# Performance work log

Measured on AMD Instinct MI355X. Metric: run time of the kernel, lower is better.

Reference implementation:

```python
import jax, jax.numpy as jnp
import numpy as np

N, F_IN, HID, NCLS, E = 100000, 256, 256, 32, 3200000
NHEADS, HDIM, MFEAT = 4, 64, 266  # MFEAT = int(HDIM * ln(HDIM)), performer default
ALPHA, KSTEPS, EPS = 0.1, 10, 1e-4


def setup_inputs() -> dict:
    key = jax.random.key(0)
    ks = jax.random.split(key, 16)
    p = lambda k, sh: (jax.random.normal(k, sh, dtype=jnp.float32) * 0.02)
    return {
        "x": jax.random.normal(ks[0], (N, F_IN), dtype=jnp.float32),
        "edge_index": jax.random.randint(ks[1], (2, E), 0, N, dtype=jnp.int64),
        "lin1_w": p(ks[2], (HID, F_IN)), "lin1_b": p(ks[3], (HID,)),
        "lin2_w": p(ks[4], (NCLS, 2 * HID)), "lin2_b": p(ks[5], (NCLS,)),
        "q_w": p(ks[6], (HID, F_IN)), "q_b": p(ks[7], (HID,)),
        "k_w": p(ks[8], (HID, F_IN)), "k_b": p(ks[9], (HID,)),
        "v_w": p(ks[10], (HID, F_IN)), "v_b": p(ks[11], (HID,)),
        "proj": jax.random.normal(ks[12], (MFEAT, HDIM), dtype=jnp.float32),
    }


def _softmax_kernel(data, proj, is_query):
    # performer_pytorch softmax random-feature map
    d = data.shape[-1]
    m = proj.shape[0]
    dn = d ** -0.25
    ratio = m ** -0.5
    data_dash = jnp.einsum('bhnd,md->bhnm', data * dn, proj)
    diag = 0.5 * (dn ** 2) * jnp.sum(data * data, axis=-1, keepdims=True)  # [b,h,n,1]
    if is_query:
        mx = jax.lax.stop_gradient(jnp.max(data_dash, axis=-1, keepdims=True))
    else:
        mx = jax.lax.stop_gradient(jnp.max(data_dash, axis=(-2, -1), keepdims=True))
    return ratio * (jnp.exp(data_dash - diag - mx) + EPS)


def _fast_attention(q, k, v, proj):
    # non-causal performer linear attention; q,k,v: [b,h,n,d]
    qp = _softmax_kernel(q, proj, True)   # [b,h,n,m]
    kp = _softmax_kernel(k, proj, False)  # [b,h,n,m]
    k_sum = jnp.sum(kp, axis=-2)                                   # [b,h,m]
    d_inv = 1.0 / jnp.einsum('bhnm,bhm->bhn', qp, k_sum)           # [b,h,n]
    context = jnp.einsum('bhnm,bhnd->bhmd', kp, v)                 # [b,h,m,d]
    return jnp.einsum('bhmd,bhnm,bhn->bhnd', context, qp, d_inv)   # [b,h,n,d]


def _appnp(x, edge_index, n):
    # gcn_norm with self-loops, then K iterations of x <- (1-a) A_hat x + a h
    src = jnp.concatenate([edge_index[0], jnp.arange(n, dtype=edge_index.dtype)])
    dst = jnp.concatenate([edge_index[1], jnp.arange(n, dtype=edge_index.dtype)])
    deg = jax.ops.segment_sum(jnp.ones_like(dst, dtype=x.dtype), dst, num_segments=n)
    dis = jnp.where(deg > 0, jax.lax.rsqrt(deg), 0.0)
    w = (dis[src] * dis[dst])[:, None]  # [E+N, 1]
    h = x
    for _ in range(KSTEPS):
        msg = jax.ops.segment_sum(x[src] * w, dst, num_segments=n)
        x = (1.0 - ALPHA) * msg + ALPHA * h
    return x


def reference(x, edge_index, lin1_w, lin1_b, lin2_w, lin2_b,
              q_w, q_b, k_w, k_b, v_w, v_b, proj):
    n = x.shape[0]
    # dropout layers are identity in eval mode
    xu = x[None]  # [1, N, F]
    q = (xu @ q_w.T + q_b).reshape(1, n, NHEADS, HDIM).transpose(0, 2, 1, 3)
    k = (xu @ k_w.T + k_b).reshape(1, n, NHEADS, HDIM).transpose(0, 2, 1, 3)
    v = (xu @ v_w.T + v_b).reshape(1, n, NHEADS, HDIM).transpose(0, 2, 1, 3)
    attn = _fast_attention(q, k, v, proj)                      # [1,h,n,d]
    trans = attn.transpose(0, 2, 1, 3).reshape(n, HID)         # [N, HID]
    gnn1 = x @ lin1_w.T + lin1_b                               # [N, HID]
    cat = jax.nn.elu(jnp.concatenate([gnn1, trans], axis=1))   # [N, 2*HID]
    gnn2 = jax.nn.elu(cat @ lin2_w.T + lin2_b)                 # [N, NCLS]
    final = _appnp(gnn2, edge_index, n)
    return jax.nn.log_softmax(final, axis=1), final
```

## Files before the change

kernel.cpp:

```cpp
#include <hip/hip_runtime.h>
#include <hip/hip_fp16.h>

#define NH 4
#define HD 64
#define MF 266
#define MP 288
#define NB 192
#define NBQ 128
#define DN 0.35355339059327373f
#define RATIO 0.06131393394849658f
#define EPSRF 1e-4f
#define REPS (RATIO*EPSRF)

typedef unsigned short u16;
typedef unsigned int u32;
typedef __attribute__((ext_vector_type(8))) short bf16x8;
typedef __attribute__((ext_vector_type(4))) float f32x4;
#define MFMA16(a,b,c) __builtin_amdgcn_mfma_f32_16x16x32_bf16(a,b,c,0,0,0)

__device__ __forceinline__ float bf2f(u16 u){ return __uint_as_float(((u32)u)<<16); }
__device__ __forceinline__ u16 f2bf(float f){ u32 u = __float_as_uint(f); u += 0x7FFFu + ((u>>16)&1u); return (u16)(u>>16); }
__device__ __forceinline__ u32 pack2bf(float a, float b){ return ((u32)f2bf(b)<<16) | f2bf(a); }
__device__ __forceinline__ float eluf(float x){ return x>0.f ? x : (expf(x)-1.f); }

__global__ void k_cvtw(const float* __restrict__ qw, const float* __restrict__ kw,
                       const float* __restrict__ vw, const float* __restrict__ lw,
                       const float* __restrict__ l2w, const float* __restrict__ proj,
                       u16* __restrict__ Wb, u16* __restrict__ projp, u16* __restrict__ l2wb){
  int i = blockIdx.x*256 + threadIdx.x;
  if (i < 262144){
    int sec = i>>16, r = i&65535;
    const float* s = sec==0?qw : sec==1?kw : sec==2?vw : lw;
    Wb[i] = f2bf(s[r]);
  }
  if (i < MP*64){
    int r = i>>6, c = i&63;
    projp[i] = f2bf(r < MF ? proj[r*64 + c] : 0.f);
  }
  if (i < 32*512) l2wb[i] = f2bf(l2w[i]);
}

__global__ __launch_bounds__(512,4) void k_proj(
    const float* __restrict__ x, const u16* __restrict__ Wb,
    const float* __restrict__ qb, const float* __restrict__ kb,
    const float* __restrict__ vb, const float* __restrict__ lb,
    u16* __restrict__ Q, u16* __restrict__ K, u16* __restrict__ V,
    u16* __restrict__ G1, int n)
{
  __shared__ u32 Xs[128*128];
  const int tid = threadIdx.x;
  const int w = tid>>6, l = tid&63;
  const int wr = w>>2, wc = w&3;
  const int lm = l&15, lk = l>>4;
  const int row0 = blockIdx.x*128;
  #pragma unroll 4
  for (int q=0;q<16;++q){
    int idx = q*512 + tid;
    int r = idx>>6, c4 = idx&63;
    int rr = row0 + r; if (rr > n-1) rr = n-1;
    float4 v = *(const float4*)(x + (size_t)rr*256 + c4*4);
    int word = (c4*2) ^ ((r&7)<<2);
    *(uint2*)&Xs[r*128 + word] = make_uint2(pack2bf(v.x,v.y), pack2bf(v.z,v.w));
  }
  __syncthreads();
  #pragma unroll 1
  for (int ct=0; ct<8; ++ct){
    const int c0 = ct*128 + wc*32;
    f32x4 acc[4][2] = {};
    #pragma unroll 2
    for (int kt=0; kt<8; ++kt){
      bf16x8 Af[4], Bf[2];
      #pragma unroll
      for (int jj=0;jj<2;jj++)
        Bf[jj] = *(const bf16x8*)(Wb + (size_t)(c0 + jj*16 + lm)*256 + kt*32 + lk*8);
      #pragma unroll
      for (int i=0;i<4;i++){
        const int rl = wr*64 + i*16 + lm;
        Af[i] = *(const bf16x8*)&Xs[rl*128 + ((kt*16 + lk*4) ^ ((rl&7)<<2))];
      }
      #pragma unroll
      for (int i=0;i<4;i++)
        #pragma unroll
        for (int jj=0;jj<2;jj++)
          acc[i][jj] = MFMA16(Af[i], Bf[jj], acc[i][jj]);
    }
    const int sel = c0>>8;
    const float* bp = sel==0?qb : sel==1?kb : sel==2?vb : lb;
    u16* d3 = sel==0?Q : sel==1?K : sel==2?V : G1;
    u32* dst32 = (u32*)d3;
    const bool even = (lm&1)==0;
    #pragma unroll
    for (int jj=0;jj<2;jj++){
      const int cc = (c0&255) + jj*16 + lm;
      const float bias = bp[cc];
      const int ccA = cc & ~1;
      const int hh = ccA>>6, dd = ccA&63;
      #pragma unroll
      for (int i=0;i<4;i++){
        const int rb = row0 + wr*64 + i*16 + lk*4;
        u32 m01 = pack2bf(acc[i][jj][0]+bias, acc[i][jj][1]+bias);
        u32 m23 = pack2bf(acc[i][jj][2]+bias, acc[i][jj][3]+bias);
        u32 oa = __shfl_xor(m01,1);
        u32 ob = __shfl_xor(m23,1);
        u32 wA = even ? ((m01 & 0xffffu) | ((oa & 0xffffu)<<16))
                      : ((ob  & 0xffffu) | ((m23 & 0xffffu)<<16));
        u32 wB = even ? ((m01 >> 16) | (oa & 0xffff0000u))
                      : ((ob  >> 16) | (m23 & 0xffff0000u));
        const int rA = rb + (even ? 0 : 2);
        const int rB = rA + 1;
        if (sel==3){
          if (rA < n) dst32[(size_t)rA*128 + (ccA>>1)] = wA;
          if (rB < n) dst32[(size_t)rB*128 + (ccA>>1)] = wB;
        } else {
          if (rA < n) dst32[(((size_t)hh*n + rA)<<5) + (dd>>1)] = wA;
          if (rB < n) dst32[(((size_t)hh*n + rB)<<5) + (dd>>1)] = wB;
        }
      }
    }
  }
}

__global__ void k_vcs(const u16* __restrict__ Vb, float* __restrict__ vcs, int n){
  const int h = blockIdx.y, tid = threadIdx.x;
  const int d = tid&63, seg = tid>>6;
  float s = 0.f;
  for (int node = blockIdx.x*4 + seg; node < n; node += 256)
    s += bf2f(Vb[(((size_t)h*n + node)<<6) + d]);
  __shared__ float sm[4][64];
  sm[seg][d] = s; __syncthreads();
  if (tid < 64){
    float t2 = sm[0][tid]+sm[1][tid]+sm[2][tid]+sm[3][tid];
    atomicAdd(vcs + h*64 + tid, t2);
  }
}

__global__ __launch_bounds__(256) void k_ctx(
    const u16* __restrict__ Kb, const u16* __restrict__ Vb,
    const u16* __restrict__ projp,
    float* __restrict__ ctxp, float* __restrict__ ksump,
    u32* __restrict__ kmaxg, int n)
{
  __shared__ u32 kpT[288*32];
  __shared__ u16 Vt[64][72];
  __shared__ float redk[4][288];
  const int tid = threadIdx.x;
  const int w = tid>>6, l = tid&63;
  const int bb = blockIdx.x;
  const int h = blockIdx.y;
  const int lm = l&15, lk = l>>4;
  f32x4 cacc[18] = {};
  float ksa[18] = {};
  float mreg = -3.0e38f;
  const int ntile = (n+63)>>6;
  #pragma unroll 1
  for (int t=bb; t<ntile; t+=NB){
    const int n0 = t*64;
    __syncthreads();
    #pragma unroll
    for (int q=0;q<2;q++){
      int e8 = tid + q*256;
      int nn = e8>>3, d0 = (e8&7)*8;
      uint4 rv = make_uint4(0,0,0,0);
      if (n0+nn < n) rv = *(const uint4*)(Vb + (((size_t)h*n + n0+nn)<<6) + d0);
      const u16* pv = (const u16*)&rv;
      #pragma unroll
      for (int s=0;s<8;s++) Vt[d0+s][nn] = pv[s];
    }
    int rr = n0 + w*16 + lm; if (rr > n-1) rr = n-1;
    const u16* Kbase = Kb + (((size_t)h*n + rr)<<6);
    bf16x8 af0 = *(const bf16x8*)(Kbase + lk*8);
    bf16x8 af1 = *(const bf16x8*)(Kbase + 32 + lk*8);
    float dg = 0.f;
    #pragma unroll
    for (int i2=0;i2<8;i2++){
      float a = bf2f(((const u16*)&af0)[i2]);
      float b = bf2f(((const u16*)&af1)[i2]);
      dg += a*a + b*b;
    }
    dg += __shfl_xor(dg,16); dg += __shfl_xor(dg,32);
    dg *= 0.0625f;
    float dgr[4];
    #pragma unroll
    for (int j=0;j<4;j++) dgr[j] = __shfl(dg, lk*4+j, 16);
    #pragma unroll
    for (int mt=0; mt<18; ++mt){
      bf16x8 b0 = *(const bf16x8*)(projp + (size_t)(mt*16+lm)*64 + lk*8);
      bf16x8 b1 = *(const bf16x8*)(projp + (size_t)(mt*16+lm)*64 + 32 + lk*8);
      f32x4 D = {0,0,0,0};
      D = MFMA16(af0, b0, D);
      D = MFMA16(af1, b1, D);
      const int m = mt*16 + lm;
      const bool vm = m < MF;
      float colsum = 0.f;
      u32 pk0 = 0, pk1 = 0;
      #pragma unroll
      for (int j=0;j<4;j++){
        float ddash = DN * D[j];
        float kp = 0.f;
        if (vm && (n0 + w*16 + lk*4 + j) < n){
          kp = RATIO * __expf(ddash - dgr[j]);
          mreg = fmaxf(mreg, ddash);
          colsum += kp;
        }
        if (j<2) pk0 |= ((u32)f2bf(kp)) << (16*j);
        else     pk1 |= ((u32)f2bf(kp)) << (16*(j-2));
      }
      const int wn0 = w*8 + lk*2;
      *(uint2*)&kpT[m*32 + (wn0 ^ ((m&7)<<2))] = make_uint2(pk0, pk1);
      colsum += __shfl_xor(colsum,16); colsum += __shfl_xor(colsum,32);
      ksa[mt] += colsum;
    }
    __syncthreads();
    #pragma unroll
    for (int mt=0; mt<18; ++mt){
      const int m = mt*16 + lm;
      #pragma unroll
      for (int ks=0;ks<2;++ks){
        bf16x8 a = *(const bf16x8*)&kpT[m*32 + ((ks*16 + lk*4) ^ ((m&7)<<2))];
        bf16x8 bv = *(const bf16x8*)&Vt[w*16+lm][ks*32 + lk*8];
        cacc[mt] = MFMA16(a, bv, cacc[mt]);
      }
    }
  }
  float* cp = ctxp + ((size_t)(h*NB + bb))*MP*64;
  #pragma unroll
  for (int mt=0;mt<18;++mt){
    #pragma unroll
    for (int j=0;j<4;j++){
      int m = mt*16 + lk*4 + j;
      cp[(size_t)m*64 + w*16 + lm] = cacc[mt][j];
    }
  }
  if (l < 16){
    #pragma unroll
    for (int mt=0;mt<18;++mt) redk[w][mt*16+lm] = ksa[mt];
  }
  __shared__ float redm[4];
  float mr = mreg;
  #pragma unroll
  for (int s=1;s<64;s<<=1) mr = fmaxf(mr, __shfl_xor(mr, s));
  if (l==0) redm[w] = mr;
  __syncthreads();
  for (int m2=tid; m2<MP; m2+=256){
    float s = redk[0][m2]+redk[1][m2]+redk[2][m2]+redk[3][m2];
    ksump[((size_t)(h*NB+bb))*MP + m2] = s;
  }
  if (tid==0){
    float bm = fmaxf(fmaxf(redm[0],redm[1]), fmaxf(redm[2],redm[3]));
    u32 b = __float_as_uint(bm);
    u32 enc = (b & 0x80000000u) ? ~b : (b | 0x80000000u);
    atomicMax(kmaxg + h, enc);
  }
}

__global__ void k_reduce(const float* __restrict__ ctxp, const float* __restrict__ ksump,
                         const u32* __restrict__ kmaxg, const float* __restrict__ vcs,
                         u16* __restrict__ ctxT, float* __restrict__ ksum, int n)
{
  const int T1 = NH*MP*64;
  int idx = blockIdx.x*256 + threadIdx.x;
  if (idx < T1){
    int h = idx/(MP*64), r = idx - h*MP*64, m = r>>6, d = r&63;
    u32 ee = kmaxg[h]; u32 b = (ee & 0x80000000u) ? (ee ^ 0x80000000u) : ~ee;
    float sc = __expf(-__uint_as_float(b));
    float s = 0.f;
    for (int bb=0; bb<NB; ++bb) s += ctxp[(((size_t)(h*NB+bb))*MP + m)*64 + d];
    float val = (m < MF) ? (sc*s + REPS*vcs[h*64 + d]) : 0.f;
    ctxT[((size_t)h*64 + d)*MP + m] = f2bf(val);
  } else if (idx < T1 + NH*MP){
    int k2 = idx - T1, h = k2/MP, m = k2 - h*MP;
    u32 ee = kmaxg[h]; u32 b = (ee & 0x80000000u) ? (ee ^ 0x80000000u) : ~ee;
    float sc = __expf(-__uint_as_float(b));
    float s = 0.f;
    for (int bb=0; bb<NB; ++bb) s += ksump[((size_t)(h*NB+bb))*MP + m];
    ksum[h*MP + m] = (m < MF) ? (sc*s + REPS*(float)n) : 0.f;
  }
}

__global__ __launch_bounds__(256) void k_qattn(
    const u16* __restrict__ Qb, const u16* __restrict__ projp,
    const u16* __restrict__ ctxT, const float* __restrict__ ksum,
    u16* __restrict__ trans, int n)
{
  __shared__ u32 pj[288*32];
  __shared__ u16 qp_lds[4][16][168];
  const int tid = threadIdx.x;
  const int w = tid>>6, l = tid&63;
  const int h = blockIdx.y;
  const int lm = l&15, lk = l>>4;
  #pragma unroll
  for (int q=0; q<9; ++q){
    int cix = q*256 + tid;
    int row = cix>>3, c4 = (cix&7)*4;
    uint4 v = *(const uint4*)(projp + row*64 + c4*2);
    *(uint4*)&pj[row*32 + (c4 ^ ((row&7)<<2))] = v;
  }
  float ksm[18];
  #pragma unroll
  for (int mt=0;mt<18;++mt) ksm[mt] = ksum[h*MP + mt*16 + lm];
  __syncthreads();
  const int ntile = (n+63)>>6;
  #pragma unroll 1
  for (int t = blockIdx.x; t < ntile; t += NBQ){
    const int nb = t*64 + w*16;
    int rr = nb + lm; if (rr > n-1) rr = n-1;
    const u16* Qbase = Qb + (((size_t)h*n + rr)<<6);
    bf16x8 af0 = *(const bf16x8*)(Qbase + lk*8);
    bf16x8 af1 = *(const bf16x8*)(Qbase + 32 + lk*8);
    float dg = 0.f;
    #pragma unroll
    for (int i2=0;i2<8;i2++){
      float a = bf2f(((const u16*)&af0)[i2]);
      float b = bf2f(((const u16*)&af1)[i2]);
      dg += a*a + b*b;
    }
    dg += __shfl_xor(dg,16); dg += __shfl_xor(dg,32);
    dg *= 0.0625f;
    float dgr[4];
    #pragma unroll
    for (int j=0;j<4;j++) dgr[j] = __shfl(dg, lk*4+j, 16);
    f32x4 D[18];
    #pragma unroll
    for (int mt=0;mt<18;++mt){
      const int m = mt*16 + lm;
      bf16x8 b0 = *(const bf16x8*)&pj[m*32 + ((lk*4) ^ ((m&7)<<2))];
      bf16x8 b1 = *(const bf16x8*)&pj[m*32 + ((16 + lk*4) ^ ((m&7)<<2))];
      f32x4 z = {0,0,0,0};
      z = MFMA16(af0, b0, z);
      z = MFMA16(af1, b1, z);
      D[mt] = z;
    }
    float rmax[4] = {-3.0e38f,-3.0e38f,-3.0e38f,-3.0e38f};
    #pragma unroll
    for (int mt=0;mt<17;++mt){
      const bool vm = (mt<16) || (lm<10);
      #pragma unroll
      for (int j=0;j<4;j++){
        float dd = DN*D[mt][j];
        if (vm) rmax[j] = fmaxf(rmax[j], dd);
      }
    }
    #pragma unroll
    for (int j=0;j<4;j++){
      #pragma unroll
      for (int s=1;s<16;s<<=1) rmax[j] = fmaxf(rmax[j], __shfl_xor(rmax[j], s));
    }
    float den[4] = {0,0,0,0};
    f32x4 o[4] = {{0,0,0,0},{0,0,0,0},{0,0,0,0},{0,0,0,0}};
    #pragma unroll
    for (int mt=0;mt<10;++mt){
      #pragma unroll
      for (int j=0;j<4;j++){
        float qp = RATIO*(__expf(DN*D[mt][j] - dgr[j] - rmax[j]) + EPSRF);
        den[j] += qp * ksm[mt];
        qp_lds[w][lk*4+j][mt*16+lm] = f2bf(qp);
      }
    }
    #pragma unroll
    for (int ks=0;ks<5;++ks){
      bf16x8 av = *(const bf16x8*)&qp_lds[w][lm][ks*32 + lk*8];
      #pragma unroll
      for (int dt=0;dt<4;++dt){
        bf16x8 bv = *(const bf16x8*)(ctxT + (size_t)(h*64 + dt*16 + lm)*MP + ks*32 + lk*8);
        o[dt] = MFMA16(av, bv, o[dt]);
      }
    }
    #pragma unroll
    for (int mt=10;mt<18;++mt){
      #pragma unroll
      for (int j=0;j<4;j++){
        float qp = RATIO*(__expf(DN*D[mt][j] - dgr[j] - rmax[j]) + EPSRF);
        den[j] += qp * ksm[mt];
        qp_lds[w][lk*4+j][(mt-10)*16+lm] = f2bf(qp);
      }
    }
    #pragma unroll
    for (int ks=5;ks<9;++ks){
      bf16x8 av = *(const bf16x8*)&qp_lds[w][lm][(ks-5)*32 + lk*8];
      #pragma unroll
      for (int dt=0;dt<4;++dt){
        bf16x8 bv = *(const bf16x8*)(ctxT + (size_t)(h*64 + dt*16 + lm)*MP + ks*32 + lk*8);
        o[dt] = MFMA16(av, bv, o[dt]);
      }
    }
    #pragma unroll
    for (int j=0;j<4;j++){
      #pragma unroll
      for (int s=1;s<16;s<<=1) den[j] += __shfl_xor(den[j], s);
    }
    #pragma unroll
    for (int j=0;j<4;j++){
      const int node = nb + lk*4 + j;
      if (node < n){
        const float dv = 1.f/den[j];
        #pragma unroll
        for (int dt=0;dt<4;++dt)
          trans[(size_t)node*256 + h*64 + dt*16 + lm] = f2bf(o[dt][j]*dv);
      }
    }
  }
}

__global__ __launch_bounds__(256) void k_gnn2(
    const u16* __restrict__ G1, const u16* __restrict__ trans,
    const u16* __restrict__ l2wb, const float* __restrict__ l2b,
    u16* __restrict__ xb0, int n)
{
  __shared__ u32 cat[64*256];
  const int tid = threadIdx.x;
  const int w = tid>>6, l = tid&63;
  const int lm = l&15, lk = l>>4;
  const int n0 = blockIdx.x*64;
  #pragma unroll
  for (int src=0; src<2; ++src){
    const u16* S = src ? trans : G1;
    #pragma unroll
    for (int q=0;q<8;++q){
      int idx = q*256 + tid;
      int row = idx>>5, v8 = idx&31;
      int rr = n0+row; if (rr > n-1) rr = n-1;
      uint4 raw = *(const uint4*)(S + (size_t)rr*256 + v8*8);
      const u16* p = (const u16*)&raw;
      u32 o2[4];
      #pragma unroll
      for (int t2=0;t2<4;++t2)
        o2[t2] = pack2bf(eluf(bf2f(p[t2*2])), eluf(bf2f(p[t2*2+1])));
      int word = (v8*4 + src*128) ^ ((row&7)<<2);
      *(uint4*)&cat[row*256 + word] = *(uint4*)o2;
    }
  }
  __syncthreads();
  f32x4 acc[2] = {{0,0,0,0},{0,0,0,0}};
  const int rowl = w*16 + lm;
  #pragma unroll 4
  for (int kt=0; kt<16; ++kt){
    bf16x8 a = *(const bf16x8*)&cat[rowl*256 + ((kt*16 + lk*4) ^ ((rowl&7)<<2))];
    #pragma unroll
    for (int jj=0;jj<2;++jj){
      bf16x8 b = *(const bf16x8*)(l2wb + (size_t)(jj*16+lm)*512 + kt*32 + lk*8);
      acc[jj] = MFMA16(a, b, acc[jj]);
    }
  }
  #pragma unroll
  for (int jj=0;jj<2;++jj){
    const int o = jj*16 + lm;
    const float bias = l2b[o];
    #pragma unroll
    for (int jr=0;jr<4;++jr){
      const int node = n0 + w*16 + lk*4 + jr;
      if (node < n)
        xb0[(size_t)node*32 + o] = f2bf(eluf(acc[jj][jr] + bias));
    }
  }
}

__global__ void k_edgemode(const int* __restrict__ ei, int* __restrict__ mode){
  __shared__ int any;
  if (threadIdx.x==0) any = 0;
  __syncthreads();
  if (ei[threadIdx.x*2+1] != 0) any = 1;
  __syncthreads();
  if (threadIdx.x==0) *mode = any;
}
__device__ __forceinline__ int edge_at(const int* ei, int mode, size_t idx){
  if (mode) return ei[idx];
  return (int)((const long long*)ei)[idx];
}

__global__ void k_hist(const int* __restrict__ ei, const int* __restrict__ mode,
                       u32* __restrict__ deg, int e){
  const int md = *mode;
  for (size_t i = (size_t)blockIdx.x*blockDim.x + threadIdx.x; i < (size_t)e; i += (size_t)gridDim.x*blockDim.x)
    atomicAdd(&deg[edge_at(ei, md, (size_t)e + i)], 1u);
}
__global__ void k_dis(const u32* __restrict__ deg, float* __restrict__ dis, int n){
  int i = blockIdx.x*256 + threadIdx.x;
  if (i<n) dis[i] = rsqrtf((float)(deg[i] + 1u));
}
__global__ __launch_bounds__(256) void k_bsum(const u32* __restrict__ deg,
                                              u32* __restrict__ bsum, int n){
  __shared__ u32 red[4];
  const int tid = threadIdx.x, lane = tid&63, wv = tid>>6;
  const int base = blockIdx.x*1024;
  u32 s = 0;
  #pragma unroll
  for (int q=0;q<4;++q){
    int i = base + q*256 + tid;
    if (i<n) s += deg[i];
  }
  #pragma unroll
  for (int off=1; off<64; off<<=1) s += __shfl_xor(s, off, 64);
  if (lane==0) red[wv] = s;
  __syncthreads();
  if (tid==0) bsum[blockIdx.x] = red[0]+red[1]+red[2]+red[3];
}
__global__ __launch_bounds__(1024) void k_bscan(u32* __restrict__ bsum,
                                                u32* __restrict__ rowp, int nblk){
  __shared__ u32 wsum[16];
  __shared__ u32 carry;
  const int tid = threadIdx.x, lane = tid&63, wv = tid>>6;
  if (tid==0){ carry = 0u; rowp[0] = 0u; }
  __syncthreads();
  for (int base=0; base<nblk; base+=1024){
    int i = base + tid;
    u32 v = (i<nblk)? bsum[i] : 0u;
    u32 s = v;
    #pragma unroll
    for (int off=1; off<64; off<<=1){
      u32 t = __shfl_up(s, off, 64);
      if (lane >= off) s += t;
    }
    if (lane==63) wsum[wv] = s;
    __syncthreads();
    if (wv==0){
      u32 ws = (lane<16)? wsum[lane] : 0u;
      #pragma unroll
      for (int off=1; off<16; off<<=1){
        u32 t = __shfl_up(ws, off, 64);
        if (lane >= off) ws += t;
      }
      if (lane<16) wsum[lane] = ws;
    }
    __syncthreads();
    if (i<nblk) bsum[i] = carry + (wv ? wsum[wv-1] : 0u) + s - v;
    __syncthreads();
    if (tid==0) carry += wsum[15];
    __syncthreads();
  }
}
__global__ __launch_bounds__(1024) void k_scan2(const u32* __restrict__ deg,
                                                const u32* __restrict__ bsum,
                                                u32* __restrict__ rowp, int n){
  __shared__ u32 wsum[16];
  const int tid = threadIdx.x, lane = tid&63, wv = tid>>6;
  const int i = blockIdx.x*1024 + tid;
  u32 v = (i<n)? deg[i] : 0u;
  u32 s = v;
  #pragma unroll
  for (int off=1; off<64; off<<=1){
    u32 t = __shfl_up(s, off, 64);
    if (lane >= off) s += t;
  }
  if (lane==63) wsum[wv] = s;
  __syncthreads();
  if (wv==0){
    u32 ws = (lane<16)? wsum[lane] : 0u;
    #pragma unroll
    for (int off=1; off<16; off<<=1){
      u32 t = __shfl_up(ws, off, 64);
      if (lane >= off) ws += t;
    }
    if (lane<16) wsum[lane] = ws;
  }
  __syncthreads();
  if (i<n) rowp[i+1] = bsum[blockIdx.x] + (wv ? wsum[wv-1] : 0u) + s;
}
__global__ void k_copy(const u32* __restrict__ a, u32* __restrict__ b, int n){
  int i = blockIdx.x*256 + threadIdx.x; if (i<n) b[i]=a[i];
}
__global__ void k_fill(const int* __restrict__ ei, const int* __restrict__ mode,
                       const float* __restrict__ dis,
                       u32* __restrict__ cur, uint2* __restrict__ cw, int e){
  const int md = *mode;
  for (size_t i = (size_t)blockIdx.x*blockDim.x + threadIdx.x; i < (size_t)e; i += (size_t)gridDim.x*blockDim.x){
    int s = edge_at(ei, md, i);
    int t = edge_at(ei, md, (size_t)e + i);
    u32 pos = atomicAdd(&cur[t], 1u);
    cw[pos] = make_uint2((u32)s, __float_as_uint(dis[s]*dis[t]));
  }
}

__global__ __launch_bounds__(256) void k_appnp(
    const u16* __restrict__ xin, const u16* __restrict__ hb16,
    u16* __restrict__ xout, const u32* __restrict__ rowp,
    const uint2* __restrict__ cw, const float* __restrict__ dis, int n)
{
  const int g = threadIdx.x>>3, j4 = threadIdx.x&7;
  const int node = blockIdx.x*32 + g;
  if (node >= n) return;
  const uint2* x64 = (const uint2*)xin;
  float d0 = dis[node];
  float dd = d0*d0;
  uint2 xv = x64[((size_t)node<<3) + j4];
  float a0 = dd*bf2f((u16)xv.x), a1 = dd*bf2f((u16)(xv.x>>16));
  float a2 = dd*bf2f((u16)xv.y), a3 = dd*bf2f((u16)(xv.y>>16));
  u32 r0 = rowp[node], r1 = rowp[node+1];
  u32 k = r0;
  for (; k+4 <= r1; k += 4){
    uint2 e0 = cw[k], e1 = cw[k+1], e2 = cw[k+2], e3 = cw[k+3];
    uint2 v0 = x64[((size_t)e0.x<<3)+j4], v1 = x64[((size_t)e1.x<<3)+j4];
    uint2 v2 = x64[((size_t)e2.x<<3)+j4], v3 = x64[((size_t)e3.x<<3)+j4];
    float w0=__uint_as_float(e0.y), w1=__uint_as_float(e1.y);
    float w2=__uint_as_float(e2.y), w3=__uint_as_float(e3.y);
    a0 += w0*bf2f((u16)v0.x) + w1*bf2f((u16)v1.x) + w2*bf2f((u16)v2.x) + w3*bf2f((u16)v3.x);
    a1 += w0*bf2f((u16)(v0.x>>16)) + w1*bf2f((u16)(v1.x>>16)) + w2*bf2f((u16)(v2.x>>16)) + w3*bf2f((u16)(v3.x>>16));
    a2 += w0*bf2f((u16)v0.y) + w1*bf2f((u16)v1.y) + w2*bf2f((u16)v2.y) + w3*bf2f((u16)v3.y);
    a3 += w0*bf2f((u16)(v0.y>>16)) + w1*bf2f((u16)(v1.y>>16)) + w2*bf2f((u16)(v2.y>>16)) + w3*bf2f((u16)(v3.y>>16));
  }
  for (; k < r1; ++k){
    uint2 e = cw[k];
    uint2 v = x64[((size_t)e.x<<3)+j4];
    float wgt = __uint_as_float(e.y);
    a0 += wgt*bf2f((u16)v.x);
    a1 += wgt*bf2f((u16)(v.x>>16));
    a2 += wgt*bf2f((u16)v.y);
    a3 += wgt*bf2f((u16)(v.y>>16));
  }
  uint2 hv = ((const uint2*)hb16)[((size_t)node<<3) + j4];
  uint2 o;
  o.x = pack2bf(0.9f*a0 + 0.1f*bf2f((u16)hv.x), 0.9f*a1 + 0.1f*bf2f((u16)(hv.x>>16)));
  o.y = pack2bf(0.9f*a2 + 0.1f*bf2f((u16)hv.y), 0.9f*a3 + 0.1f*bf2f((u16)(hv.y>>16)));
  ((uint2*)xout)[((size_t)node<<3) + j4] = o;
}

__global__ __launch_bounds__(256) void k_appnp_lsm(
    const u16* __restrict__ xin, const u16* __restrict__ hb16,
    float* __restrict__ out, const u32* __restrict__ rowp,
    const uint2* __restrict__ cw, const float* __restrict__ dis, int n)
{
  const int g = threadIdx.x>>3, j4 = threadIdx.x&7;
  const int node = blockIdx.x*32 + g;
  if (node >= n) return;
  const uint2* x64 = (const uint2*)xin;
  float d0 = dis[node];
  float dd = d0*d0;
  uint2 xv = x64[((size_t)node<<3) + j4];
  float a0 = dd*bf2f((u16)xv.x), a1 = dd*bf2f((u16)(xv.x>>16));
  float a2 = dd*bf2f((u16)xv.y), a3 = dd*bf2f((u16)(xv.y>>16));
  u32 r0 = rowp[node], r1 = rowp[node+1];
  u32 k = r0;
  for (; k+4 <= r1; k += 4){
    uint2 e0 = cw[k], e1 = cw[k+1], e2 = cw[k+2], e3 = cw[k+3];
    uint2 v0 = x64[((size_t)e0.x<<3)+j4], v1 = x64[((size_t)e1.x<<3)+j4];
    uint2 v2 = x64[((size_t)e2.x<<3)+j4], v3 = x64[((size_t)e3.x<<3)+j4];
    float w0=__uint_as_float(e0.y), w1=__uint_as_float(e1.y);
    float w2=__uint_as_float(e2.y), w3=__uint_as_float(e3.y);
    a0 += w0*bf2f((u16)v0.x) + w1*bf2f((u16)v1.x) + w2*bf2f((u16)v2.x) + w3*bf2f((u16)v3.x);
    a1 += w0*bf2f((u16)(v0.x>>16)) + w1*bf2f((u16)(v1.x>>16)) + w2*bf2f((u16)(v2.x>>16)) + w3*bf2f((u16)(v3.x>>16));
    a2 += w0*bf2f((u16)v0.y) + w1*bf2f((u16)v1.y) + w2*bf2f((u16)v2.y) + w3*bf2f((u16)v3.y);
    a3 += w0*bf2f((u16)(v0.y>>16)) + w1*bf2f((u16)(v1.y>>16)) + w2*bf2f((u16)(v2.y>>16)) + w3*bf2f((u16)(v3.y>>16));
  }
  for (; k < r1; ++k){
    uint2 e = cw[k];
    uint2 v = x64[((size_t)e.x<<3)+j4];
    float wgt = __uint_as_float(e.y);
    a0 += wgt*bf2f((u16)v.x);
    a1 += wgt*bf2f((u16)(v.x>>16));
    a2 += wgt*bf2f((u16)v.y);
    a3 += wgt*bf2f((u16)(v.y>>16));
  }
  uint2 hv = ((const uint2*)hb16)[((size_t)node<<3) + j4];
  float v0 = 0.9f*a0 + 0.1f*bf2f((u16)hv.x);
  float v1 = 0.9f*a1 + 0.1f*bf2f((u16)(hv.x>>16));
  float v2 = 0.9f*a2 + 0.1f*bf2f((u16)hv.y);
  float v3 = 0.9f*a3 + 0.1f*bf2f((u16)(hv.y>>16));
  float m = fmaxf(fmaxf(v0,v1), fmaxf(v2,v3));
  #pragma unroll
  for (int o2=1;o2<8;o2<<=1) m = fmaxf(m, __shfl_xor(m, o2, 8));
  float s = __expf(v0-m)+__expf(v1-m)+__expf(v2-m)+__expf(v3-m);
  #pragma unroll
  for (int o2=1;o2<8;o2<<=1) s += __shfl_xor(s, o2, 8);
  float ls = m + logf(s);
  float4 lsv = make_float4(v0-ls, v1-ls, v2-ls, v3-ls);
  *(float4*)(out + (size_t)node*32 + j4*4) = lsv;
  float4 raw = make_float4(v0, v1, v2, v3);
  *(float4*)(out + (size_t)n*32 + (size_t)node*32 + j4*4) = raw;
}

extern "C" void kernel_launch(void* const* d_in, const int* in_sizes, int n_in,
                              void* d_out, int out_size, void* d_ws, size_t ws_size,
                              hipStream_t stream)
{
  const float* x   = (const float*)d_in[0];
  const int*   ei  = (const int*)  d_in[1];
  const float* l1w = (const float*)d_in[2];
  const float* l1b = (const float*)d_in[3];
  const float* l2w = (const float*)d_in[4];
  const float* l2b = (const float*)d_in[5];
  const float* qw  = (const float*)d_in[6];
  const float* qb  = (const float*)d_in[7];
  const float* kw  = (const float*)d_in[8];
  const float* kb  = (const float*)d_in[9];
  const float* vw  = (const float*)d_in[10];
  const float* vb  = (const float*)d_in[11];
  const float* proj= (const float*)d_in[12];
  const int n = in_sizes[0] / 256;
  const int e = in_sizes[1] / 2;

  char* ws = (char*)d_ws;
  auto au = [](size_t v){ return (v + 255) & ~(size_t)255; };
  const size_t bQ = (size_t)n * 512;
  const size_t oQ = 0;
  const size_t oK = au(oQ + bQ);
  const size_t oV = au(oK + bQ);
  const size_t oG1 = au(oV + bQ);
  const size_t oCtxp = au(oG1 + bQ);
  const size_t bCtxp = (size_t)NH*NB*MP*64*4;
  const size_t oKsump = au(oCtxp + bCtxp);
  const size_t bKsump = (size_t)NH*NB*MP*4;
  const size_t oCtxT = au(oKsump + bKsump);
  const size_t oKsum = au(oCtxT + (size_t)NH*64*MP*2);
  const size_t oKmax = au(oKsum + (size_t)NH*MP*4);
  const size_t oVcs  = oKmax + 256;
  const size_t oMode = oVcs + 1024;
  const size_t oL2wb = au(oMode + 256);
  const size_t oWb   = au(oL2wb + 32768);
  const size_t oProjp= au(oWb + (size_t)1024*256*2);
  const size_t oTrans = oK;
  const size_t oG2 = oQ;
  const size_t oXb0 = au(oG2 + (size_t)n*32*4);
  const size_t oXbA = au(oXb0 + (size_t)n*32*2);
  const size_t oXbB = au(oXbA + (size_t)n*32*2);
  const size_t oDeg = au(oXbB + (size_t)n*32*2);
  const size_t oDis = au(oDeg + (size_t)n*4);
  const size_t oRowp= au(oDis + (size_t)n*4);
  const size_t oCur = au(oRowp + (size_t)(n+1)*4);
  const size_t oBsum= au(oCur + (size_t)(n+1)*4);
  const size_t oCw  = oV;
  (void)ws_size; (void)n_in; (void)out_size;

  u16* Q  = (u16*)(ws + oQ);
  u16* Kb = (u16*)(ws + oK);
  u16* Vb = (u16*)(ws + oV);
  u16* G1 = (u16*)(ws + oG1);
  float* ctxp = (float*)(ws + oCtxp);
  float* ksump= (float*)(ws + oKsump);
  u16*  ctxT  = (u16*)(ws + oCtxT);
  float* ksum = (float*)(ws + oKsum);
  u32*  kmax  = (u32*)(ws + oKmax);
  float* Vcs  = (float*)(ws + oVcs);
  int*  mode  = (int*)(ws + oMode);
  u16*  l2wb  = (u16*)(ws + oL2wb);
  u16*  Wb    = (u16*)(ws + oWb);
  u16*  projp = (u16*)(ws + oProjp);
  u16* trans  = (u16*)(ws + oTrans);
  u16* xb0    = (u16*)(ws + oXb0);
  u16* xbA    = (u16*)(ws + oXbA);
  u16* xbB    = (u16*)(ws + oXbB);
  u32* deg    = (u32*)(ws + oDeg);
  float* dis  = (float*)(ws + oDis);
  u32* rowp   = (u32*)(ws + oRowp);
  u32* cur    = (u32*)(ws + oCur);
  u32* bsum   = (u32*)(ws + oBsum);
  uint2* cw   = (uint2*)(ws + oCw);

  k_cvtw<<<1024,256,0,stream>>>(qw,kw,vw,l1w,l2w,proj,Wb,projp,l2wb);
  k_proj<<<(n+127)/128,512,0,stream>>>(x,Wb,qb,kb,vb,l1b,Q,Kb,Vb,G1,n);
  hipMemsetAsync(ws + oKmax, 0, 16, stream);
  hipMemsetAsync(ws + oVcs, 0, 1024, stream);
  k_vcs<<<dim3(64,4),256,0,stream>>>(Vb,Vcs,n);
  k_ctx<<<dim3(NB,NH),256,0,stream>>>(Kb,Vb,projp,ctxp,ksump,kmax,n);
  {
    int tot = NH*MP*64 + NH*MP;
    k_reduce<<<(tot+255)/256,256,0,stream>>>(ctxp,ksump,kmax,Vcs,ctxT,ksum,n);
  }
  k_qattn<<<dim3(NBQ,4),256,0,stream>>>(Q,projp,ctxT,ksum,trans,n);
  k_gnn2<<<(n+63)/64,256,0,stream>>>(G1,trans,l2wb,l2b,xb0,n);
  k_edgemode<<<1,256,0,stream>>>(ei,mode);
  hipMemsetAsync(ws + oDeg, 0, (size_t)n*4, stream);
  k_hist<<<2048,256,0,stream>>>(ei,mode,deg,e);
  k_dis<<<(n+255)/256,256,0,stream>>>(deg,dis,n);
  {
    const int nblk = (n+1023)/1024;
    k_bsum<<<nblk,256,0,stream>>>(deg,bsum,n);
    k_bscan<<<1,1024,0,stream>>>(bsum,rowp,nblk);
    k_scan2<<<nblk,1024,0,stream>>>(deg,bsum,rowp,n);
  }
  k_copy<<<(n+255)/256,256,0,stream>>>(rowp,cur,n);
  k_fill<<<2048,256,0,stream>>>(ei,mode,dis,cur,cw,e);
  const u16* curx = xb0;
  u16* bufs[2] = {xbA, xbB};
  for (int it=0; it<9; ++it){
    u16* nxt = bufs[it&1];
    k_appnp<<<(n+31)/32,256,0,stream>>>(curx,xb0,nxt,rowp,cw,dis,n);
    curx = nxt;
  }
  k_appnp_lsm<<<(n+31)/32,256,0,stream>>>(curx,xb0,(float*)d_out,rowp,cw,dis,n);
}
```

Before: 1.404 ms.

## Split APPNP propagation into two 16-feature halves to shrink gather working set

Splits the 32-wide bf16 propagation state into two 16-column halves, each stored as its own 3.2MB array, and runs all ten APPNP iterations for one half before the other. Log-softmax moves into a separate final kernel. This is meant to keep each gathered feature array small enough to stay cache-resident during the random-neighbor gathers. The cost is that the CSR edge list is streamed twice as often (20 passes instead of 10), with nontemporal loads used so those edge reads do not evict the features. It also folds the cur-pointer copy into the scan kernel, removing one launch.

```diff
diff --git a/kernel.cpp b/kernel.cpp
--- a/kernel.cpp
+++ b/kernel.cpp
@@ -14,6 +14,7 @@
 
 typedef unsigned short u16;
 typedef unsigned int u32;
+typedef unsigned long long u64;
 typedef __attribute__((ext_vector_type(8))) short bf16x8;
 typedef __attribute__((ext_vector_type(4))) float f32x4;
 #define MFMA16(a,b,c) __builtin_amdgcn_mfma_f32_16x16x32_bf16(a,b,c,0,0,0)
@@ -404,7 +405,7 @@
 __global__ __launch_bounds__(256) void k_gnn2(
     const u16* __restrict__ G1, const u16* __restrict__ trans,
     const u16* __restrict__ l2wb, const float* __restrict__ l2b,
-    u16* __restrict__ xb0, int n)
+    u16* __restrict__ h0, u16* __restrict__ h1, int n)
 {
   __shared__ u32 cat[64*256];
   const int tid = threadIdx.x;
@@ -445,11 +446,12 @@
   for (int jj=0;jj<2;++jj){
     const int o = jj*16 + lm;
     const float bias = l2b[o];
+    u16* hb = jj ? h1 : h0;
     #pragma unroll
     for (int jr=0;jr<4;++jr){
       const int node = n0 + w*16 + lk*4 + jr;
       if (node < n)
-        xb0[(size_t)node*32 + o] = f2bf(eluf(acc[jj][jr] + bias));
+        hb[(size_t)node*16 + lm] = f2bf(eluf(acc[jj][jr] + bias));
     }
   }
 }
@@ -530,7 +532,8 @@
 }
 __global__ __launch_bounds__(1024) void k_scan2(const u32* __restrict__ deg,
                                                 const u32* __restrict__ bsum,
-                                                u32* __restrict__ rowp, int n){
+                                                u32* __restrict__ rowp,
+                                                u32* __restrict__ cur, int n){
   __shared__ u32 wsum[16];
   const int tid = threadIdx.x, lane = tid&63, wv = tid>>6;
   const int i = blockIdx.x*1024 + tid;
@@ -553,10 +556,11 @@
     if (lane<16) wsum[lane] = ws;
   }
   __syncthreads();
-  if (i<n) rowp[i+1] = bsum[blockIdx.x] + (wv ? wsum[wv-1] : 0u) + s;
-}
-__global__ void k_copy(const u32* __restrict__ a, u32* __restrict__ b, int n){
-  int i = blockIdx.x*256 + threadIdx.x; if (i<n) b[i]=a[i];
+  if (i<n){
+    u32 inc = bsum[blockIdx.x] + (wv ? wsum[wv-1] : 0u) + s;
+    rowp[i+1] = inc;
+    cur[i] = inc - v;
+  }
 }
 __global__ void k_fill(const int* __restrict__ ei, const int* __restrict__ mode,
                        const float* __restrict__ dis,
@@ -570,101 +574,72 @@
   }
 }
 
-__global__ __launch_bounds__(256) void k_appnp(
-    const u16* __restrict__ xin, const u16* __restrict__ hb16,
+__global__ __launch_bounds__(256) void k_appnp_h(
+    const u16* __restrict__ xin, const u16* __restrict__ hb,
     u16* __restrict__ xout, const u32* __restrict__ rowp,
     const uint2* __restrict__ cw, const float* __restrict__ dis, int n)
 {
-  const int g = threadIdx.x>>3, j4 = threadIdx.x&7;
+  const int g = threadIdx.x>>3, j = threadIdx.x&7;
   const int node = blockIdx.x*32 + g;
   if (node >= n) return;
-  const uint2* x64 = (const uint2*)xin;
+  const u32* x32 = (const u32*)xin;
+  const u64* cw64 = (const u64*)cw;
   float d0 = dis[node];
   float dd = d0*d0;
-  uint2 xv = x64[((size_t)node<<3) + j4];
-  float a0 = dd*bf2f((u16)xv.x), a1 = dd*bf2f((u16)(xv.x>>16));
-  float a2 = dd*bf2f((u16)xv.y), a3 = dd*bf2f((u16)(xv.y>>16));
+  u32 xv = x32[(size_t)node*8 + j];
+  float a0 = dd*bf2f((u16)xv), a1 = dd*bf2f((u16)(xv>>16));
   u32 r0 = rowp[node], r1 = rowp[node+1];
   u32 k = r0;
   for (; k+4 <= r1; k += 4){
-    uint2 e0 = cw[k], e1 = cw[k+1], e2 = cw[k+2], e3 = cw[k+3];
-    uint2 v0 = x64[((size_t)e0.x<<3)+j4], v1 = x64[((size_t)e1.x<<3)+j4];
-    uint2 v2 = x64[((size_t)e2.x<<3)+j4], v3 = x64[((size_t)e3.x<<3)+j4];
-    float w0=__uint_as_float(e0.y), w1=__uint_as_float(e1.y);
-    float w2=__uint_as_float(e2.y), w3=__uint_as_float(e3.y);
-    a0 += w0*bf2f((u16)v0.x) + w1*bf2f((u16)v1.x) + w2*bf2f((u16)v2.x) + w3*bf2f((u16)v3.x);
-    a1 += w0*bf2f((u16)(v0.x>>16)) + w1*bf2f((u16)(v1.x>>16)) + w2*bf2f((u16)(v2.x>>16)) + w3*bf2f((u16)(v3.x>>16));
-    a2 += w0*bf2f((u16)v0.y) + w1*bf2f((u16)v1.y) + w2*bf2f((u16)v2.y) + w3*bf2f((u16)v3.y);
-    a3 += w0*bf2f((u16)(v0.y>>16)) + w1*bf2f((u16)(v1.y>>16)) + w2*bf2f((u16)(v2.y>>16)) + w3*bf2f((u16)(v3.y>>16));
+    u64 e0 = __builtin_nontemporal_load(cw64 + k);
+    u64 e1 = __builtin_nontemporal_load(cw64 + k + 1);
+    u64 e2 = __builtin_nontemporal_load(cw64 + k + 2);
+    u64 e3 = __builtin_nontemporal_load(cw64 + k + 3);
+    u32 v0 = x32[((size_t)(u32)e0)*8 + j];
+    u32 v1 = x32[((size_t)(u32)e1)*8 + j];
+    u32 v2 = x32[((size_t)(u32)e2)*8 + j];
+    u32 v3 = x32[((size_t)(u32)e3)*8 + j];
+    float w0 = __uint_as_float((u32)(e0>>32));
+    float w1 = __uint_as_float((u32)(e1>>32));
+    float w2 = __uint_as_float((u32)(e2>>32));
+    float w3 = __uint_as_float((u32)(e3>>32));
+    a0 += w0*bf2f((u16)v0) + w1*bf2f((u16)v1) + w2*bf2f((u16)v2) + w3*bf2f((u16)v3);
+    a1 += w0*bf2f((u16)(v0>>16)) + w1*bf2f((u16)(v1>>16)) + w2*bf2f((u16)(v2>>16)) + w3*bf2f((u16)(v3>>16));
   }
   for (; k < r1; ++k){
-    uint2 e = cw[k];
-    uint2 v = x64[((size_t)e.x<<3)+j4];
-    float wgt = __uint_as_float(e.y);
-    a0 += wgt*bf2f((u16)v.x);
-    a1 += wgt*bf2f((u16)(v.x>>16));
-    a2 += wgt*bf2f((u16)v.y);
-    a3 += wgt*bf2f((u16)(v.y>>16));
-  }
-  uint2 hv = ((const uint2*)hb16)[((size_t)node<<3) + j4];
-  uint2 o;
-  o.x = pack2bf(0.9f*a0 + 0.1f*bf2f((u16)hv.x), 0.9f*a1 + 0.1f*bf2f((u16)(hv.x>>16)));
-  o.y = pack2bf(0.9f*a2 + 0.1f*bf2f((u16)hv.y), 0.9f*a3 + 0.1f*bf2f((u16)(hv.y>>16)));
-  ((uint2*)xout)[((size_t)node<<3) + j4] = o;
-}
-
-__global__ __launch_bounds__(256) void k_appnp_lsm(
-    const u16* __restrict__ xin, const u16* __restrict__ hb16,
-    float* __restrict__ out, const u32* __restrict__ rowp,
-    const uint2* __restrict__ cw, const float* __restrict__ dis, int n)
+    u64 e = __builtin_nontemporal_load(cw64 + k);
+    u32 v = x32[((size_t)(u32)e)*8 + j];
+    float wgt = __uint_as_float((u32)(e>>32));
+    a0 += wgt*bf2f((u16)v);
+    a1 += wgt*bf2f((u16)(v>>16));
+  }
+  u32 hv = __builtin_nontemporal_load((const u32*)hb + (size_t)node*8 + j);
+  ((u32*)xout)[(size_t)node*8 + j] =
+      pack2bf(0.9f*a0 + 0.1f*bf2f((u16)hv), 0.9f*a1 + 0.1f*bf2f((u16)(hv>>16)));
+}
+
+__global__ __launch_bounds__(256) void k_lsm2(
+    const u16* __restrict__ x0, const u16* __restrict__ x1,
+    float* __restrict__ out, int n)
 {
-  const int g = threadIdx.x>>3, j4 = threadIdx.x&7;
+  const int g = threadIdx.x>>3, j = threadIdx.x&7;
   const int node = blockIdx.x*32 + g;
   if (node >= n) return;
-  const uint2* x64 = (const uint2*)xin;
-  float d0 = dis[node];
-  float dd = d0*d0;
-  uint2 xv = x64[((size_t)node<<3) + j4];
-  float a0 = dd*bf2f((u16)xv.x), a1 = dd*bf2f((u16)(xv.x>>16));
-  float a2 = dd*bf2f((u16)xv.y), a3 = dd*bf2f((u16)(xv.y>>16));
-  u32 r0 = rowp[node], r1 = rowp[node+1];
-  u32 k = r0;
-  for (; k+4 <= r1; k += 4){
-    uint2 e0 = cw[k], e1 = cw[k+1], e2 = cw[k+2], e3 = cw[k+3];
-    uint2 v0 = x64[((size_t)e0.x<<3)+j4], v1 = x64[((size_t)e1.x<<3)+j4];
-    uint2 v2 = x64[((size_t)e2.x<<3)+j4], v3 = x64[((size_t)e3.x<<3)+j4];
-    float w0=__uint_as_float(e0.y), w1=__uint_as_float(e1.y);
-    float w2=__uint_as_float(e2.y), w3=__uint_as_float(e3.y);
-    a0 += w0*bf2f((u16)v0.x) + w1*bf2f((u16)v1.x) + w2*bf2f((u16)v2.x) + w3*bf2f((u16)v3.x);
-    a1 += w0*bf2f((u16)(v0.x>>16)) + w1*bf2f((u16)(v1.x>>16)) + w2*bf2f((u16)(v2.x>>16)) + w3*bf2f((u16)(v3.x>>16));
-    a2 += w0*bf2f((u16)v0.y) + w1*bf2f((u16)v1.y) + w2*bf2f((u16)v2.y) + w3*bf2f((u16)v3.y);
-    a3 += w0*bf2f((u16)(v0.y>>16)) + w1*bf2f((u16)(v1.y>>16)) + w2*bf2f((u16)(v2.y>>16)) + w3*bf2f((u16)(v3.y>>16));
-  }
-  for (; k < r1; ++k){
-    uint2 e = cw[k];
-    uint2 v = x64[((size_t)e.x<<3)+j4];
-    float wgt = __uint_as_float(e.y);
-    a0 += wgt*bf2f((u16)v.x);
-    a1 += wgt*bf2f((u16)(v.x>>16));
-    a2 += wgt*bf2f((u16)v.y);
-    a3 += wgt*bf2f((u16)(v.y>>16));
-  }
-  uint2 hv = ((const uint2*)hb16)[((size_t)node<<3) + j4];
-  float v0 = 0.9f*a0 + 0.1f*bf2f((u16)hv.x);
-  float v1 = 0.9f*a1 + 0.1f*bf2f((u16)(hv.x>>16));
-  float v2 = 0.9f*a2 + 0.1f*bf2f((u16)hv.y);
-  float v3 = 0.9f*a3 + 0.1f*bf2f((u16)(hv.y>>16));
-  float m = fmaxf(fmaxf(v0,v1), fmaxf(v2,v3));
+  u32 a = ((const u32*)x0)[(size_t)node*8 + j];
+  u32 b = ((const u32*)x1)[(size_t)node*8 + j];
+  float va0 = bf2f((u16)a), va1 = bf2f((u16)(a>>16));
+  float vb0 = bf2f((u16)b), vb1 = bf2f((u16)(b>>16));
+  float m = fmaxf(fmaxf(va0,va1), fmaxf(vb0,vb1));
   #pragma unroll
   for (int o2=1;o2<8;o2<<=1) m = fmaxf(m, __shfl_xor(m, o2, 8));
-  float s = __expf(v0-m)+__expf(v1-m)+__expf(v2-m)+__expf(v3-m);
+  float s = __expf(va0-m)+__expf(va1-m)+__expf(vb0-m)+__expf(vb1-m);
   #pragma unroll
   for (int o2=1;o2<8;o2<<=1) s += __shfl_xor(s, o2, 8);
   float ls = m + logf(s);
-  float4 lsv = make_float4(v0-ls, v1-ls, v2-ls, v3-ls);
-  *(float4*)(out + (size_t)node*32 + j4*4) = lsv;
-  float4 raw = make_float4(v0, v1, v2, v3);
-  *(float4*)(out + (size_t)n*32 + (size_t)node*32 + j4*4) = raw;
+  *(float2*)(out + (size_t)node*32 + 2*j)      = make_float2(va0-ls, va1-ls);
+  *(float2*)(out + (size_t)node*32 + 16 + 2*j) = make_float2(vb0-ls, vb1-ls);
+  *(float2*)(out + (size_t)n*32 + (size_t)node*32 + 2*j)      = make_float2(va0, va1);
+  *(float2*)(out + (size_t)n*32 + (size_t)node*32 + 16 + 2*j) = make_float2(vb0, vb1);
 }
 
 extern "C" void kernel_launch(void* const* d_in, const int* in_sizes, int n_in,
@@ -708,10 +683,13 @@
   const size_t oProjp= au(oWb + (size_t)1024*256*2);
   const size_t oTrans = oK;
   const size_t oG2 = oQ;
-  const size_t oXb0 = au(oG2 + (size_t)n*32*4);
-  const size_t oXbA = au(oXb0 + (size_t)n*32*2);
-  const size_t oXbB = au(oXbA + (size_t)n*32*2);
-  const size_t oDeg = au(oXbB + (size_t)n*32*2);
+  const size_t oH0 = au(oG2 + (size_t)n*32*4);
+  const size_t oH1 = au(oH0 + (size_t)n*32);
+  const size_t oA0 = au(oH1 + (size_t)n*32);
+  const size_t oA1 = au(oA0 + (size_t)n*32);
+  const size_t oB0 = au(oA1 + (size_t)n*32);
+  const size_t oB1 = au(oB0 + (size_t)n*32);
+  const size_t oDeg = au(oB1 + (size_t)n*32);
   const size_t oDis = au(oDeg + (size_t)n*4);
   const size_t oRowp= au(oDis + (size_t)n*4);
   const size_t oCur = au(oRowp + (size_t)(n+1)*4);
@@ -734,9 +712,9 @@
   u16*  Wb    = (u16*)(ws + oWb);
   u16*  projp = (u16*)(ws + oProjp);
   u16* trans  = (u16*)(ws + oTrans);
-  u16* xb0    = (u16*)(ws + oXb0);
-  u16* xbA    = (u16*)(ws + oXbA);
-  u16* xbB    = (u16*)(ws + oXbB);
+  u16* H[2]   = {(u16*)(ws + oH0), (u16*)(ws + oH1)};
+  u16* PA[2]  = {(u16*)(ws + oA0), (u16*)(ws + oA1)};
+  u16* PB[2]  = {(u16*)(ws + oB0), (u16*)(ws + oB1)};
   u32* deg    = (u32*)(ws + oDeg);
   float* dis  = (float*)(ws + oDis);
   u32* rowp   = (u32*)(ws + oRowp);
@@ -755,7 +733,7 @@
     k_reduce<<<(tot+255)/256,256,0,stream>>>(ctxp,ksump,kmax,Vcs,ctxT,ksum,n);
   }
   k_qattn<<<dim3(NBQ,4),256,0,stream>>>(Q,projp,ctxT,ksum,trans,n);
-  k_gnn2<<<(n+63)/64,256,0,stream>>>(G1,trans,l2wb,l2b,xb0,n);
+  k_gnn2<<<(n+63)/64,256,0,stream>>>(G1,trans,l2wb,l2b,H[0],H[1],n);
   k_edgemode<<<1,256,0,stream>>>(ei,mode);
   hipMemsetAsync(ws + oDeg, 0, (size_t)n*4, stream);
   k_hist<<<2048,256,0,stream>>>(ei,mode,deg,e);
@@ -764,16 +742,18 @@
     const int nblk = (n+1023)/1024;
     k_bsum<<<nblk,256,0,stream>>>(deg,bsum,n);
     k_bscan<<<1,1024,0,stream>>>(bsum,rowp,nblk);
-    k_scan2<<<nblk,1024,0,stream>>>(deg,bsum,rowp,n);
-  }
-  k_copy<<<(n+255)/256,256,0,stream>>>(rowp,cur,n);
+    k_scan2<<<nblk,1024,0,stream>>>(deg,bsum,rowp,cur,n);
+  }
   k_fill<<<2048,256,0,stream>>>(ei,mode,dis,cur,cw,e);
-  const u16* curx = xb0;
-  u16* bufs[2] = {xbA, xbB};
-  for (int it=0; it<9; ++it){
-    u16* nxt = bufs[it&1];
-    k_appnp<<<(n+31)/32,256,0,stream>>>(curx,xb0,nxt,rowp,cw,dis,n);
-    curx = nxt;
-  }
-  k_appnp_lsm<<<(n+31)/32,256,0,stream>>>(curx,xb0,(float*)d_out,rowp,cw,dis,n);
-}
+  const u16* fin[2];
+  for (int h=0; h<2; ++h){
+    const u16* curx = H[h];
+    for (int it=0; it<10; ++it){
+      u16* nxt = (it&1) ? PB[h] : PA[h];
+      k_appnp_h<<<(n+31)/32,256,0,stream>>>(curx,H[h],nxt,rowp,cw,dis,n);
+      curx = nxt;
+    }
+    fin[h] = curx;
+  }
+  k_lsm2<<<(n+31)/32,256,0,stream>>>(fin[0],fin[1],(float*)d_out,n);
+}
```

After: 1.949 ms. 38.8% more time.
